# Kernel tuning notes

Measured on AMD Instinct MI355X. Metric: run time of the kernel, lower is better.

## Reference

```python
import jax, jax.numpy as jnp
import numpy as np

OUT_IMG = 256
OUT_MSK = 64


def _src_coords(n_out, size):
    # F.interpolate bilinear align_corners=False source coordinates, clamped to edge
    sizef = size.astype(jnp.float32)
    t = (jnp.arange(n_out, dtype=jnp.float32) + 0.5) * (sizef / n_out) - 0.5
    t = jnp.clip(t, 0.0, sizef - 1.0)
    t0 = jnp.floor(t).astype(jnp.int32)
    t1 = jnp.minimum(t0 + 1, size - 1)
    return t0, t1, t - t0.astype(jnp.float32)


def _per_sample(x_img, x_msk, x_bg, pad, sel, color):
    # x_img [3,H,W] float, x_msk [H,W] bool, x_bg [3,Hb,Wb], pad [4] int (l,r,t,b)
    H, W = x_msk.shape
    ys = jnp.any(x_msk, axis=1)
    xs = jnp.any(x_msk, axis=0)
    iy = jnp.arange(H)
    ix = jnp.arange(W)
    miny = jnp.min(jnp.where(ys, iy, H))
    maxy = jnp.max(jnp.where(ys, iy, -1))
    minx = jnp.min(jnp.where(xs, ix, W))
    maxx = jnp.max(jnp.where(xs, ix, -1))
    h = maxy - miny + 1
    w = maxx - minx + 1
    left, right, top, bot = pad[0], pad[1], pad[2], pad[3]
    Hp = h + top + bot   # padded crop height
    Wp = w + left + right  # padded crop width
    # background: real bg image or solid random color (c[ii][-1] > 2 branch)
    bg_sel = jnp.where(sel > 2, x_bg, jnp.broadcast_to(color[:, None, None], x_bg.shape))

    def mask_at(P, Q):
        # value of the padded-cropped mask at integer padded coords (P, Q)
        in_crop = (P >= top) & (P < top + h) & (Q >= left) & (Q < left + w)
        r = jnp.clip(miny + P - top, 0, H - 1)
        c = jnp.clip(minx + Q - left, 0, W - 1)
        return in_crop & x_msk[r, c], r, c

    def sample_img(py, px):
        # composited padded image at integer coords (py x px grid) -> [3,Ho,Wo]
        P = py[:, None]
        Q = px[None, :]
        m, r, c = mask_at(P, Q)
        iv = x_img[:, r, c]
        bv = bg_sel[:, P, Q]
        return jnp.where(m[None], iv, bv)

    def sample_msk(py, px):
        m, _, _ = mask_at(py[:, None], px[None, :])
        return m.astype(jnp.float32)

    def bilinear(sample_fn, n_out, ch_leading):
        y0, y1, wy = _src_coords(n_out, Hp)
        x0, x1, wx = _src_coords(n_out, Wp)
        s00 = sample_fn(y0, x0)
        s01 = sample_fn(y0, x1)
        s10 = sample_fn(y1, x0)
        s11 = sample_fn(y1, x1)
        wy_ = wy[:, None]
        wx_ = wx[None, :]
        if ch_leading:
            wy_ = wy_[None]
            wx_ = wx_[None]
        top_row = s00 * (1.0 - wx_) + s01 * wx_
        bot_row = s10 * (1.0 - wx_) + s11 * wx_
        return top_row * (1.0 - wy_) + bot_row * wy_

    img_out = bilinear(sample_img, OUT_IMG, True)        # [3,256,256]
    msk_out = bilinear(sample_msk, OUT_MSK, False)[None]  # [1,64,64]
    return img_out, msk_out


def _rgb_to_hsv(x):
    r, g, b = x[:, 0], x[:, 1], x[:, 2]
    mx = jnp.max(x, axis=1)
    mn = jnp.min(x, axis=1)
    d = mx - mn
    ds = jnp.where(d > 0, d, 1.0)
    hr = ((g - b) / ds) % 6.0
    hg = (b - r) / ds + 2.0
    hb = (r - g) / ds + 4.0
    hch = jnp.where(mx == r, hr, jnp.where(mx == g, hg, hb)) / 6.0
    hch = jnp.where(d > 0, hch, 0.0)
    s = jnp.where(mx > 0, d / jnp.where(mx > 0, mx, 1.0), 0.0)
    return hch, s, mx


def _hsv_to_rgb(hch, s, v):
    h6 = hch * 6.0
    i = jnp.floor(h6)
    f = h6 - i
    p = v * (1.0 - s)
    q = v * (1.0 - f * s)
    t = v * (1.0 - (1.0 - f) * s)
    im = i.astype(jnp.int32) % 6
    conds = [im == 0, im == 1, im == 2, im == 3, im == 4, im == 5]
    r = jnp.select(conds, [v, q, p, p, t, v])
    g = jnp.select(conds, [t, v, v, q, p, p])
    b = jnp.select(conds, [p, p, t, v, v, q])
    return jnp.stack([r, g, b], axis=1)


def _color_jitter(img, jit):
    # ColorJitter(0.1, 0.1, 0.1, 0.1) with explicit per-sample factors
    b = (0.9 + 0.2 * jit[:, 0])[:, None, None, None]
    c = (0.9 + 0.2 * jit[:, 1])[:, None, None, None]
    s = (0.9 + 0.2 * jit[:, 2])[:, None, None, None]
    hd = (-0.1 + 0.2 * jit[:, 3])[:, None, None]
    img = jnp.clip(img * b, 0.0, 1.0)
    gray = (0.299 * img[:, 0] + 0.587 * img[:, 1] + 0.114 * img[:, 2])[:, None]
    mean = jnp.mean(gray, axis=(2, 3), keepdims=True)
    img = jnp.clip(c * img + (1.0 - c) * mean, 0.0, 1.0)
    gray = (0.299 * img[:, 0] + 0.587 * img[:, 1] + 0.114 * img[:, 2])[:, None]
    img = jnp.clip(s * img + (1.0 - s) * gray, 0.0, 1.0)
    hch, sa, v = _rgb_to_hsv(img)
    hch = (hch + hd) % 1.0
    return jnp.clip(_hsv_to_rgb(hch, sa, v), 0.0, 1.0)


def setup_inputs() -> dict:
    key = jax.random.key(0)
    ks = jax.random.split(key, 7)
    B, H, W = 64, 448, 448
    return {
        "img": jax.random.uniform(ks[0], (B, 3, H, W), jnp.float32),
        "ms": jax.random.uniform(ks[1], (B, 1, H, W), jnp.float32),
        "bg": jax.random.uniform(ks[2], (B, 3, H + 40, W + 40), jnp.float32),
        "pads": jax.random.randint(ks[3], (B, 4), 0, 20, jnp.int32),
        "csel": jax.random.randint(ks[4], (B,), 0, 20, jnp.int32),
        "rand_color": jax.random.uniform(ks[5], (B, 3), jnp.float32),
        "jitter": jax.random.uniform(ks[6], (B, 4), jnp.float32),
    }


def reference(img, ms, bg, pads, csel, rand_color, jitter):
    mask = ms[:, 0] > 0.5
    img_out, msk_out = jax.vmap(_per_sample)(img, mask, bg, pads, csel, rand_color)
    img_out = _color_jitter(img_out, jitter)
    return img_out, msk_out
```

## Files before the change

### kernel.cpp

```cpp
#include <hip/hip_runtime.h>

#define H_IN 448
#define W_IN 448
#define HW_IN (H_IN * W_IN)
#define BGW 488
#define BGHW (BGW * BGW)
#define OUTI 256
#define OUTI_PIX (OUTI * OUTI)
#define OUTM 64
#define B_SAMPLES 64
#define BBOX_CHUNKS 16
#define BBOX_ROWS (H_IN / BBOX_CHUNKS)

__device__ __forceinline__ float clamp01(float x) { return fminf(fmaxf(x, 0.f), 1.f); }
__device__ __forceinline__ int clampi(int x, int lo, int hi) { return min(max(x, lo), hi); }

__global__ void k_bbox(const float* __restrict__ ms, int* __restrict__ bbox) {
    int b = blockIdx.y;
    int chunk = blockIdx.x;
    const float4* m4 = (const float4*)(ms + (size_t)b * HW_IN + (size_t)chunk * BBOX_ROWS * W_IN);
    int miny = H_IN, maxy = -1, minx = W_IN, maxx = -1;
    const int N4 = BBOX_ROWS * (W_IN / 4);
    for (int i = threadIdx.x; i < N4; i += blockDim.x) {
        float4 v = m4[i];
        bool a0 = v.x > 0.5f, a1 = v.y > 0.5f, a2 = v.z > 0.5f, a3 = v.w > 0.5f;
        if (a0 | a1 | a2 | a3) {
            int y = chunk * BBOX_ROWS + i / (W_IN / 4);
            int xb = (i % (W_IN / 4)) * 4;
            miny = min(miny, y); maxy = max(maxy, y);
            if (a0) { minx = min(minx, xb);     maxx = max(maxx, xb); }
            if (a1) { minx = min(minx, xb + 1); maxx = max(maxx, xb + 1); }
            if (a2) { minx = min(minx, xb + 2); maxx = max(maxx, xb + 2); }
            if (a3) { minx = min(minx, xb + 3); maxx = max(maxx, xb + 3); }
        }
    }
    __shared__ int s[4];
    if (threadIdx.x == 0) { s[0] = H_IN; s[1] = -1; s[2] = W_IN; s[3] = -1; }
    __syncthreads();
    atomicMin(&s[0], miny); atomicMax(&s[1], maxy);
    atomicMin(&s[2], minx); atomicMax(&s[3], maxx);
    __syncthreads();
    if (threadIdx.x == 0) {
        atomicMin(&bbox[b * 4 + 0], s[0]);
        atomicMin(&bbox[b * 4 + 1], -s[1]);
        atomicMin(&bbox[b * 4 + 2], s[2]);
        atomicMin(&bbox[b * 4 + 3], -s[3]);
    }
}

struct Geo {
    int miny, minx, h, w, top, left, Hp, Wp;
};
__device__ __forceinline__ Geo load_geo(const int* __restrict__ bbox,
                                        const int* __restrict__ pads, int b) {
    Geo g;
    g.miny = bbox[b * 4 + 0];
    int maxy = -bbox[b * 4 + 1];
    g.minx = bbox[b * 4 + 2];
    int maxx = -bbox[b * 4 + 3];
    int left = pads[b * 4 + 0], right = pads[b * 4 + 1];
    int top = pads[b * 4 + 2], bot = pads[b * 4 + 3];
    g.h = maxy - g.miny + 1;
    g.w = maxx - g.minx + 1;
    g.top = top; g.left = left;
    g.Hp = g.h + top + bot;
    g.Wp = g.w + left + right;
    return g;
}

__device__ __forceinline__ void src_coord(int i, int n_out, int size,
                                          int& t0, int& t1, float& frac) {
    float sizef = (float)size;
    float t = (i + 0.5f) * (sizef / (float)n_out) - 0.5f;
    t = fminf(fmaxf(t, 0.f), sizef - 1.f);
    t0 = (int)floorf(t);
    t1 = min(t0 + 1, size - 1);
    frac = t - (float)t0;
}

__global__ void __launch_bounds__(256) k_resize_img(
        const float* __restrict__ img, const float* __restrict__ ms,
        const float* __restrict__ bg, const int* __restrict__ pads,
        const int* __restrict__ csel, const float* __restrict__ rcol,
        const float* __restrict__ jit, const int* __restrict__ bbox,
        float* __restrict__ out, float* __restrict__ partials) {
    int b = blockIdx.y;
    int oy = blockIdx.x;
    int tid = threadIdx.x;

    Geo g = load_geo(bbox, pads, b);
    bool useBg = csel[b] > 2;
    float c0 = rcol[b * 3 + 0], c1 = rcol[b * 3 + 1], c2 = rcol[b * 3 + 2];
    float bfac = 0.9f + 0.2f * jit[b * 4 + 0];

    int y0, y1; float wy;
    src_coord(oy, OUTI, g.Hp, y0, y1, wy);
    int r0 = clampi(g.miny + y0 - g.top, 0, H_IN - 1);
    int r1 = clampi(g.miny + y1 - g.top, 0, H_IN - 1);
    int P0 = clampi(y0, 0, BGW - 1);
    int P1 = clampi(y1, 0, BGW - 1);
    bool incy0 = (y0 >= g.top) && (y0 < g.top + g.h);
    bool incy1 = (y1 >= g.top) && (y1 < g.top + g.h);

    __shared__ float s_ms[2][W_IN];
    __shared__ float s_im[2][3][W_IN];
    __shared__ float s_bg[2][3][BGW];

    const float* msB = ms + (size_t)b * HW_IN;
    const float* imB = img + (size_t)b * 3 * HW_IN;
    const float* bgB = bg + (size_t)b * 3 * BGHW;

    for (int item = tid; item < 8 * (W_IN / 4); item += 256) {
        int plane = item / (W_IN / 4);
        int idx = item - plane * (W_IN / 4);
        const float* sp;
        float* dp;
        if (plane < 2) {
            sp = msB + (size_t)(plane ? r1 : r0) * W_IN;
            dp = s_ms[plane];
        } else {
            int q = plane - 2;
            int ky = q / 3, ch = q - 3 * ky;
            sp = imB + (size_t)ch * HW_IN + (size_t)(ky ? r1 : r0) * W_IN;
            dp = &s_im[ky][ch][0];
        }
        ((float4*)dp)[idx] = ((const float4*)sp)[idx];
    }
    if (useBg) {
        for (int item = tid; item < 6 * (BGW / 4); item += 256) {
            int plane = item / (BGW / 4);
            int idx = item - plane * (BGW / 4);
            int ky = plane / 3, ch = plane - 3 * ky;
            const float* sp = bgB + (size_t)ch * BGHW + (size_t)(ky ? P1 : P0) * BGW;
            ((float4*)(&s_bg[ky][ch][0]))[idx] = ((const float4*)sp)[idx];
        }
    }
    __syncthreads();

    int x0, x1; float wx;
    src_coord(tid, OUTI, g.Wp, x0, x1, wx);

    float acc0 = 0.f, acc1 = 0.f, acc2 = 0.f;
#pragma unroll
    for (int tap = 0; tap < 4; ++tap) {
        int ky = tap >> 1;
        int Q = (tap & 1) ? x1 : x0;
        float wgt = (ky ? wy : 1.f - wy) * ((tap & 1) ? wx : 1.f - wx);
        bool incy = ky ? incy1 : incy0;
        bool in_crop = incy && (Q >= g.left) && (Q < g.left + g.w);
        int c = clampi(g.minx + Q - g.left, 0, W_IN - 1);
        bool mm = in_crop && (s_ms[ky][c] > 0.5f);
        float v0, v1, v2;
        if (mm) {
            v0 = s_im[ky][0][c]; v1 = s_im[ky][1][c]; v2 = s_im[ky][2][c];
        } else if (useBg) {
            int Qc = clampi(Q, 0, BGW - 1);
            v0 = s_bg[ky][0][Qc]; v1 = s_bg[ky][1][Qc]; v2 = s_bg[ky][2][Qc];
        } else {
            v0 = c0; v1 = c1; v2 = c2;
        }
        acc0 += wgt * v0; acc1 += wgt * v1; acc2 += wgt * v2;
    }
    float o0 = clamp01(acc0 * bfac);
    float o1 = clamp01(acc1 * bfac);
    float o2 = clamp01(acc2 * bfac);
    size_t o = (size_t)b * 3 * OUTI_PIX + (size_t)oy * OUTI + tid;
    out[o] = o0;
    out[o + OUTI_PIX] = o1;
    out[o + 2 * OUTI_PIX] = o2;

    float gsum = 0.299f * o0 + 0.587f * o1 + 0.114f * o2;
#pragma unroll
    for (int off = 32; off > 0; off >>= 1) gsum += __shfl_down(gsum, off, 64);
    __shared__ float ls[4];
    int wid = tid >> 6, lane = tid & 63;
    if (lane == 0) ls[wid] = gsum;
    __syncthreads();
    if (tid == 0)
        partials[b * 256 + oy] = ls[0] + ls[1] + ls[2] + ls[3];
}

__global__ void k_resize_msk(const float* __restrict__ ms, const int* __restrict__ pads,
                             const int* __restrict__ bbox, float* __restrict__ outm) {
    int b = blockIdx.y;
    int pix = blockIdx.x * blockDim.x + threadIdx.x;
    int oy = pix >> 6, ox = pix & 63;

    Geo g = load_geo(bbox, pads, b);
    int y0, y1, x0, x1; float wy, wx;
    src_coord(oy, OUTM, g.Hp, y0, y1, wy);
    src_coord(ox, OUTM, g.Wp, x0, x1, wx);

    const float* msB = ms + (size_t)b * HW_IN;
    float acc = 0.f;
#pragma unroll
    for (int tap = 0; tap < 4; ++tap) {
        int P = (tap & 2) ? y1 : y0;
        int Q = (tap & 1) ? x1 : x0;
        float wgt = ((tap & 2) ? wy : 1.f - wy) * ((tap & 1) ? wx : 1.f - wx);
        bool in_crop = (P >= g.top) && (P < g.top + g.h) && (Q >= g.left) && (Q < g.left + g.w);
        int r = clampi(g.miny + P - g.top, 0, H_IN - 1);
        int c = clampi(g.minx + Q - g.left, 0, W_IN - 1);
        bool mm = in_crop && (msB[r * W_IN + c] > 0.5f);
        acc += wgt * (mm ? 1.f : 0.f);
    }
    outm[(size_t)b * (OUTM * OUTM) + pix] = acc;
}

__device__ __forceinline__ void jitter_px(float& r, float& g, float& bl,
                                          float cc, float ssf, float hd, float mean) {
    r = clamp01(cc * r + (1.f - cc) * mean);
    g = clamp01(cc * g + (1.f - cc) * mean);
    bl = clamp01(cc * bl + (1.f - cc) * mean);
    float gray = 0.299f * r + 0.587f * g + 0.114f * bl;
    r = clamp01(ssf * r + (1.f - ssf) * gray);
    g = clamp01(ssf * g + (1.f - ssf) * gray);
    bl = clamp01(ssf * bl + (1.f - ssf) * gray);
    float mx = fmaxf(r, fmaxf(g, bl));
    float mn = fminf(r, fminf(g, bl));
    float d = mx - mn;
    float dsv = (d > 0.f) ? d : 1.f;
    float hch;
    if (mx == r) {
        float t = (g - bl) / dsv;
        t = fmodf(t, 6.f);
        if (t < 0.f) t += 6.f;
        hch = t;
    } else if (mx == g) {
        hch = (bl - r) / dsv + 2.f;
    } else {
        hch = (r - g) / dsv + 4.f;
    }
    hch = (d > 0.f) ? hch * (1.f / 6.f) : 0.f;
    float sat = (mx > 0.f) ? d / mx : 0.f;
    float v = mx;
    float hh = hch + hd;
    hh -= floorf(hh);
    float h6 = hh * 6.f;
    float fi = floorf(h6);
    float f = h6 - fi;
    float pp = v * (1.f - sat);
    float q = v * (1.f - f * sat);
    float t = v * (1.f - (1.f - f) * sat);
    int im = ((int)fi) % 6;
    float ro, go, bo;
    switch (im) {
        case 0: ro = v;  go = t;  bo = pp; break;
        case 1: ro = q;  go = v;  bo = pp; break;
        case 2: ro = pp; go = v;  bo = t;  break;
        case 3: ro = pp; go = q;  bo = v;  break;
        case 4: ro = t;  go = pp; bo = v;  break;
        default: ro = v; go = pp; bo = q;  break;
    }
    r = clamp01(ro); g = clamp01(go); bl = clamp01(bo);
}

__global__ void k_jitter(float* __restrict__ io, const float* __restrict__ jit,
                         const float* __restrict__ partials) {
    int b = blockIdx.y;
    int tid = threadIdx.x;

    float pv = partials[b * 256 + tid];
#pragma unroll
    for (int off = 32; off > 0; off >>= 1) pv += __shfl_down(pv, off, 64);
    __shared__ float ls[4];
    int wid = tid >> 6, lane = tid & 63;
    if (lane == 0) ls[wid] = pv;
    __syncthreads();
    float mean = (ls[0] + ls[1] + ls[2] + ls[3]) * (1.f / (float)OUTI_PIX);

    float cc = 0.9f + 0.2f * jit[b * 4 + 1];
    float ssf = 0.9f + 0.2f * jit[b * 4 + 2];
    float hd = -0.1f + 0.2f * jit[b * 4 + 3];

    int idx4 = blockIdx.x * blockDim.x + tid;
    float4* pr = (float4*)(io + (size_t)b * 3 * OUTI_PIX) + idx4;
    float4* pg = pr + OUTI_PIX / 4;
    float4* pb = pr + 2 * (OUTI_PIX / 4);
    float4 r = *pr, g = *pg, bl = *pb;

    jitter_px(r.x, g.x, bl.x, cc, ssf, hd, mean);
    jitter_px(r.y, g.y, bl.y, cc, ssf, hd, mean);
    jitter_px(r.z, g.z, bl.z, cc, ssf, hd, mean);
    jitter_px(r.w, g.w, bl.w, cc, ssf, hd, mean);

    *pr = r; *pg = g; *pb = bl;
}

extern "C" void kernel_launch(void* const* d_in, const int* in_sizes, int n_in,
                              void* d_out, int out_size, void* d_ws, size_t ws_size,
                              hipStream_t stream) {
    const float* img = (const float*)d_in[0];
    const float* ms = (const float*)d_in[1];
    const float* bg = (const float*)d_in[2];
    const int* pads = (const int*)d_in[3];
    const int* csel = (const int*)d_in[4];
    const float* rcol = (const float*)d_in[5];
    const float* jit = (const float*)d_in[6];
    float* out = (float*)d_out;

    int* bbox = (int*)d_ws;
    float* partials = (float*)((char*)d_ws + B_SAMPLES * 4 * sizeof(int));
    float* outm = out + (size_t)B_SAMPLES * 3 * OUTI_PIX;

    hipMemsetAsync(bbox, 0x7F, B_SAMPLES * 4 * sizeof(int), stream);

    k_bbox<<<dim3(BBOX_CHUNKS, B_SAMPLES), 256, 0, stream>>>(ms, bbox);
    k_resize_img<<<dim3(OUTI, B_SAMPLES), 256, 0, stream>>>(
        img, ms, bg, pads, csel, rcol, jit, bbox, out, partials);
    k_resize_msk<<<dim3((OUTM * OUTM) / 256, B_SAMPLES), 256, 0, stream>>>(ms, pads, bbox, outm);
    k_jitter<<<dim3(OUTI_PIX / 4 / 256, B_SAMPLES), 256, 0, stream>>>(out, jit, partials);
}
```

Baseline: 134.6 us.

## Pack mask into bitsets during bbox pass and split resize blocks per channel

The bbox kernel now also writes a packed per-row bitmask of the thresholded mask using wave ballots. The image and mask resize kernels read those bits instead of the float mask rows. The image resize kernel is split into one block per colour channel, which triples the grid and cuts per-block shared memory and loads. The grayscale partial sums are kept per channel and weighted in the jitter kernel. This adds a bits buffer in workspace and extra small writes in the bbox pass, but removes reloading of float mask rows.

```diff
diff --git a/kernel.cpp b/kernel.cpp
--- a/kernel.cpp
+++ b/kernel.cpp
@@ -11,36 +11,56 @@
 #define B_SAMPLES 64
 #define BBOX_CHUNKS 16
 #define BBOX_ROWS (H_IN / BBOX_CHUNKS)
+#define BITS_STRIDE 8
+
+typedef unsigned long long u64;
 
 __device__ __forceinline__ float clamp01(float x) { return fminf(fmaxf(x, 0.f), 1.f); }
 __device__ __forceinline__ int clampi(int x, int lo, int hi) { return min(max(x, lo), hi); }
 
-__global__ void k_bbox(const float* __restrict__ ms, int* __restrict__ bbox) {
-    int b = blockIdx.y;
-    int chunk = blockIdx.x;
-    const float4* m4 = (const float4*)(ms + (size_t)b * HW_IN + (size_t)chunk * BBOX_ROWS * W_IN);
+__global__ void k_bbox(const float* __restrict__ ms, int* __restrict__ bbox,
+                       u64* __restrict__ bits) {
+    int b = blockIdx.y, chunk = blockIdx.x;
+    int tid = threadIdx.x;
+    int wave = tid >> 6, lane = tid & 63;
+    const float* msB = ms + (size_t)b * HW_IN;
+    u64* bitsB = bits + (size_t)b * H_IN * BITS_STRIDE;
+
     int miny = H_IN, maxy = -1, minx = W_IN, maxx = -1;
-    const int N4 = BBOX_ROWS * (W_IN / 4);
-    for (int i = threadIdx.x; i < N4; i += blockDim.x) {
-        float4 v = m4[i];
-        bool a0 = v.x > 0.5f, a1 = v.y > 0.5f, a2 = v.z > 0.5f, a3 = v.w > 0.5f;
-        if (a0 | a1 | a2 | a3) {
-            int y = chunk * BBOX_ROWS + i / (W_IN / 4);
-            int xb = (i % (W_IN / 4)) * 4;
-            miny = min(miny, y); maxy = max(maxy, y);
-            if (a0) { minx = min(minx, xb);     maxx = max(maxx, xb); }
-            if (a1) { minx = min(minx, xb + 1); maxx = max(maxx, xb + 1); }
-            if (a2) { minx = min(minx, xb + 2); maxx = max(maxx, xb + 2); }
-            if (a3) { minx = min(minx, xb + 3); maxx = max(maxx, xb + 3); }
+    for (int rr = wave; rr < BBOX_ROWS; rr += 4) {
+        int row = chunk * BBOX_ROWS + rr;
+        const float4* rowp = (const float4*)(msB + (size_t)row * W_IN);
+#pragma unroll
+        for (int sub = 0; sub < 2; ++sub) {
+            int c4 = sub * 64 + lane;
+            bool valid = c4 < (W_IN / 4);
+            float4 v = rowp[min(c4, W_IN / 4 - 1)];
+            bool a0 = valid && (v.x > 0.5f);
+            bool a1 = valid && (v.y > 0.5f);
+            bool a2 = valid && (v.z > 0.5f);
+            bool a3 = valid && (v.w > 0.5f);
+            u64 b0 = __ballot(a0), b1 = __ballot(a1), b2 = __ballot(a2), b3 = __ballot(a3);
+            if (a0 | a1 | a2 | a3) {
+                miny = min(miny, row); maxy = max(maxy, row);
+                int xb = c4 * 4;
+                if (a0) { minx = min(minx, xb);     maxx = max(maxx, xb); }
+                if (a1) { minx = min(minx, xb + 1); maxx = max(maxx, xb + 1); }
+                if (a2) { minx = min(minx, xb + 2); maxx = max(maxx, xb + 2); }
+                if (a3) { minx = min(minx, xb + 3); maxx = max(maxx, xb + 3); }
+            }
+            if (lane < 4) {
+                u64 w = (lane == 0) ? b0 : (lane == 1) ? b1 : (lane == 2) ? b2 : b3;
+                bitsB[(size_t)row * BITS_STRIDE + sub * 4 + lane] = w;
+            }
         }
     }
     __shared__ int s[4];
-    if (threadIdx.x == 0) { s[0] = H_IN; s[1] = -1; s[2] = W_IN; s[3] = -1; }
+    if (tid == 0) { s[0] = H_IN; s[1] = -1; s[2] = W_IN; s[3] = -1; }
     __syncthreads();
     atomicMin(&s[0], miny); atomicMax(&s[1], maxy);
     atomicMin(&s[2], minx); atomicMax(&s[3], maxx);
     __syncthreads();
-    if (threadIdx.x == 0) {
+    if (tid == 0) {
         atomicMin(&bbox[b * 4 + 0], s[0]);
         atomicMin(&bbox[b * 4 + 1], -s[1]);
         atomicMin(&bbox[b * 4 + 2], s[2]);
@@ -78,69 +98,64 @@
     frac = t - (float)t0;
 }
 
+__device__ __forceinline__ bool mask_bit(const u64* rowbits, int c) {
+    u64 w = rowbits[((c >> 8) << 2) | (c & 3)];
+    return (w >> ((c >> 2) & 63)) & 1ULL;
+}
+
 __global__ void __launch_bounds__(256) k_resize_img(
-        const float* __restrict__ img, const float* __restrict__ ms,
-        const float* __restrict__ bg, const int* __restrict__ pads,
-        const int* __restrict__ csel, const float* __restrict__ rcol,
-        const float* __restrict__ jit, const int* __restrict__ bbox,
+        const float* __restrict__ img, const float* __restrict__ bg,
+        const int* __restrict__ pads, const int* __restrict__ csel,
+        const float* __restrict__ rcol, const float* __restrict__ jit,
+        const int* __restrict__ bbox, const u64* __restrict__ bits,
         float* __restrict__ out, float* __restrict__ partials) {
-    int b = blockIdx.y;
     int oy = blockIdx.x;
+    int ch = blockIdx.y;
+    int b = blockIdx.z;
     int tid = threadIdx.x;
 
     Geo g = load_geo(bbox, pads, b);
     bool useBg = csel[b] > 2;
-    float c0 = rcol[b * 3 + 0], c1 = rcol[b * 3 + 1], c2 = rcol[b * 3 + 2];
+    float colv = rcol[b * 3 + ch];
     float bfac = 0.9f + 0.2f * jit[b * 4 + 0];
 
     int y0, y1; float wy;
     src_coord(oy, OUTI, g.Hp, y0, y1, wy);
     int r0 = clampi(g.miny + y0 - g.top, 0, H_IN - 1);
     int r1 = clampi(g.miny + y1 - g.top, 0, H_IN - 1);
-    int P0 = clampi(y0, 0, BGW - 1);
-    int P1 = clampi(y1, 0, BGW - 1);
     bool incy0 = (y0 >= g.top) && (y0 < g.top + g.h);
     bool incy1 = (y1 >= g.top) && (y1 < g.top + g.h);
 
-    __shared__ float s_ms[2][W_IN];
-    __shared__ float s_im[2][3][W_IN];
-    __shared__ float s_bg[2][3][BGW];
-
-    const float* msB = ms + (size_t)b * HW_IN;
-    const float* imB = img + (size_t)b * 3 * HW_IN;
-    const float* bgB = bg + (size_t)b * 3 * BGHW;
-
-    for (int item = tid; item < 8 * (W_IN / 4); item += 256) {
-        int plane = item / (W_IN / 4);
-        int idx = item - plane * (W_IN / 4);
-        const float* sp;
-        float* dp;
-        if (plane < 2) {
-            sp = msB + (size_t)(plane ? r1 : r0) * W_IN;
-            dp = s_ms[plane];
-        } else {
-            int q = plane - 2;
-            int ky = q / 3, ch = q - 3 * ky;
-            sp = imB + (size_t)ch * HW_IN + (size_t)(ky ? r1 : r0) * W_IN;
-            dp = &s_im[ky][ch][0];
-        }
-        ((float4*)dp)[idx] = ((const float4*)sp)[idx];
-    }
-    if (useBg) {
-        for (int item = tid; item < 6 * (BGW / 4); item += 256) {
-            int plane = item / (BGW / 4);
-            int idx = item - plane * (BGW / 4);
-            int ky = plane / 3, ch = plane - 3 * ky;
-            const float* sp = bgB + (size_t)ch * BGHW + (size_t)(ky ? P1 : P0) * BGW;
-            ((float4*)(&s_bg[ky][ch][0]))[idx] = ((const float4*)sp)[idx];
-        }
+    __shared__ float s_im[2][W_IN];
+    __shared__ float s_bg[2][BGW];
+    __shared__ u64 s_bits[2][BITS_STRIDE];
+
+    const float* imC = img + ((size_t)b * 3 + ch) * HW_IN;
+    const float* bgC = bg + ((size_t)b * 3 + ch) * BGHW;
+    const u64* bitsB = bits + (size_t)b * H_IN * BITS_STRIDE;
+
+    if (tid < 2 * (W_IN / 4)) {
+        int ky = tid >= (W_IN / 4);
+        int c4 = tid - ky * (W_IN / 4);
+        ((float4*)s_im[ky])[c4] =
+            ((const float4*)(imC + (size_t)(ky ? r1 : r0) * W_IN))[c4];
+    }
+    if (useBg && tid < 2 * (BGW / 4)) {
+        int ky = tid >= (BGW / 4);
+        int c4 = tid - ky * (BGW / 4);
+        ((float4*)s_bg[ky])[c4] =
+            ((const float4*)(bgC + (size_t)(ky ? y1 : y0) * BGW))[c4];
+    }
+    if (tid < 16) {
+        int ky = tid >> 3, idx = tid & 7;
+        s_bits[ky][idx] = bitsB[(size_t)(ky ? r1 : r0) * BITS_STRIDE + idx];
     }
     __syncthreads();
 
     int x0, x1; float wx;
     src_coord(tid, OUTI, g.Wp, x0, x1, wx);
 
-    float acc0 = 0.f, acc1 = 0.f, acc2 = 0.f;
+    float acc = 0.f;
 #pragma unroll
     for (int tap = 0; tap < 4; ++tap) {
         int ky = tap >> 1;
@@ -149,27 +164,14 @@
         bool incy = ky ? incy1 : incy0;
         bool in_crop = incy && (Q >= g.left) && (Q < g.left + g.w);
         int c = clampi(g.minx + Q - g.left, 0, W_IN - 1);
-        bool mm = in_crop && (s_ms[ky][c] > 0.5f);
-        float v0, v1, v2;
-        if (mm) {
-            v0 = s_im[ky][0][c]; v1 = s_im[ky][1][c]; v2 = s_im[ky][2][c];
-        } else if (useBg) {
-            int Qc = clampi(Q, 0, BGW - 1);
-            v0 = s_bg[ky][0][Qc]; v1 = s_bg[ky][1][Qc]; v2 = s_bg[ky][2][Qc];
-        } else {
-            v0 = c0; v1 = c1; v2 = c2;
-        }
-        acc0 += wgt * v0; acc1 += wgt * v1; acc2 += wgt * v2;
-    }
-    float o0 = clamp01(acc0 * bfac);
-    float o1 = clamp01(acc1 * bfac);
-    float o2 = clamp01(acc2 * bfac);
-    size_t o = (size_t)b * 3 * OUTI_PIX + (size_t)oy * OUTI + tid;
-    out[o] = o0;
-    out[o + OUTI_PIX] = o1;
-    out[o + 2 * OUTI_PIX] = o2;
-
-    float gsum = 0.299f * o0 + 0.587f * o1 + 0.114f * o2;
+        bool mm = in_crop && mask_bit(s_bits[ky], c);
+        float v = mm ? s_im[ky][c] : (useBg ? s_bg[ky][Q] : colv);
+        acc += wgt * v;
+    }
+    float o = clamp01(acc * bfac);
+    out[((size_t)b * 3 + ch) * OUTI_PIX + (size_t)oy * OUTI + tid] = o;
+
+    float gsum = o;
 #pragma unroll
     for (int off = 32; off > 0; off >>= 1) gsum += __shfl_down(gsum, off, 64);
     __shared__ float ls[4];
@@ -177,10 +179,10 @@
     if (lane == 0) ls[wid] = gsum;
     __syncthreads();
     if (tid == 0)
-        partials[b * 256 + oy] = ls[0] + ls[1] + ls[2] + ls[3];
-}
-
-__global__ void k_resize_msk(const float* __restrict__ ms, const int* __restrict__ pads,
+        partials[((size_t)b * 3 + ch) * 256 + oy] = ls[0] + ls[1] + ls[2] + ls[3];
+}
+
+__global__ void k_resize_msk(const u64* __restrict__ bits, const int* __restrict__ pads,
                              const int* __restrict__ bbox, float* __restrict__ outm) {
     int b = blockIdx.y;
     int pix = blockIdx.x * blockDim.x + threadIdx.x;
@@ -191,7 +193,7 @@
     src_coord(oy, OUTM, g.Hp, y0, y1, wy);
     src_coord(ox, OUTM, g.Wp, x0, x1, wx);
 
-    const float* msB = ms + (size_t)b * HW_IN;
+    const u64* bitsB = bits + (size_t)b * H_IN * BITS_STRIDE;
     float acc = 0.f;
 #pragma unroll
     for (int tap = 0; tap < 4; ++tap) {
@@ -201,7 +203,7 @@
         bool in_crop = (P >= g.top) && (P < g.top + g.h) && (Q >= g.left) && (Q < g.left + g.w);
         int r = clampi(g.miny + P - g.top, 0, H_IN - 1);
         int c = clampi(g.minx + Q - g.left, 0, W_IN - 1);
-        bool mm = in_crop && (msB[r * W_IN + c] > 0.5f);
+        bool mm = in_crop && mask_bit(bitsB + (size_t)r * BITS_STRIDE, c);
         acc += wgt * (mm ? 1.f : 0.f);
     }
     outm[(size_t)b * (OUTM * OUTM) + pix] = acc;
@@ -260,7 +262,9 @@
     int b = blockIdx.y;
     int tid = threadIdx.x;
 
-    float pv = partials[b * 256 + tid];
+    float pv = 0.299f * partials[((size_t)b * 3 + 0) * 256 + tid]
+             + 0.587f * partials[((size_t)b * 3 + 1) * 256 + tid]
+             + 0.114f * partials[((size_t)b * 3 + 2) * 256 + tid];
 #pragma unroll
     for (int off = 32; off > 0; off >>= 1) pv += __shfl_down(pv, off, 64);
     __shared__ float ls[4];
@@ -300,14 +304,16 @@
     float* out = (float*)d_out;
 
     int* bbox = (int*)d_ws;
-    float* partials = (float*)((char*)d_ws + B_SAMPLES * 4 * sizeof(int));
+    float* partials = (float*)((char*)d_ws + 1024);
+    u64* bits = (u64*)((char*)d_ws + 1024 + B_SAMPLES * 3 * 256 * sizeof(float));
     float* outm = out + (size_t)B_SAMPLES * 3 * OUTI_PIX;
 
     hipMemsetAsync(bbox, 0x7F, B_SAMPLES * 4 * sizeof(int), stream);
 
-    k_bbox<<<dim3(BBOX_CHUNKS, B_SAMPLES), 256, 0, stream>>>(ms, bbox);
-    k_resize_img<<<dim3(OUTI, B_SAMPLES), 256, 0, stream>>>(
-        img, ms, bg, pads, csel, rcol, jit, bbox, out, partials);
-    k_resize_msk<<<dim3((OUTM * OUTM) / 256, B_SAMPLES), 256, 0, stream>>>(ms, pads, bbox, outm);
+    k_bbox<<<dim3(BBOX_CHUNKS, B_SAMPLES), 256, 0, stream>>>(ms, bbox, bits);
+    k_resize_img<<<dim3(OUTI, 3, B_SAMPLES), 256, 0, stream>>>(
+        img, bg, pads, csel, rcol, jit, bbox, bits, out, partials);
+    k_resize_msk<<<dim3((OUTM * OUTM) / 256, B_SAMPLES), 256, 0, stream>>>(
+        bits, pads, bbox, outm);
     k_jitter<<<dim3(OUTI_PIX / 4 / 256, B_SAMPLES), 256, 0, stream>>>(out, jit, partials);
 }
```

Result: slower. 146.2 us (+8.6%).
